# Kernel tuning notes

Hardware: AMD Instinct MI355X
Metric: run time of the kernel (lower is better)

Reference implementation:

```python
import jax, jax.numpy as jnp
import numpy as np

B, S, D, H = 4, 2048, 1024, 16
DH = D // H


def setup_inputs() -> dict:
    key = jax.random.key(0)
    ks = jax.random.split(key, 11)
    s = 1.0 / np.sqrt(D)
    return {
        "q": jax.random.normal(ks[0], (B, S, D), jnp.float32),
        "k": jax.random.normal(ks[1], (B, S, D), jnp.float32),
        "v": jax.random.normal(ks[2], (B, S, D), jnp.float32),
        "Wq": jax.random.normal(ks[3], (D, D), jnp.float32) * s,
        "bq": jnp.zeros((D,), jnp.float32),
        "Wk": jax.random.normal(ks[4], (D, D), jnp.float32) * s,
        "bk": jnp.zeros((D,), jnp.float32),
        "Wv": jax.random.normal(ks[5], (D, D), jnp.float32) * s,
        "bv": jnp.zeros((D,), jnp.float32),
        "Wo": jax.random.normal(ks[6], (D, D), jnp.float32) * s,
        "bo": jnp.zeros((D,), jnp.float32),
    }


def _split_heads(x):
    # (B, S, D) -> (B, H, S, DH)
    b, s, _ = x.shape
    return x.reshape(b, s, H, DH).transpose(0, 2, 1, 3)


def reference(q, k, v, Wq, bq, Wk, bk, Wv, bv, Wo, bo):
    # torch Linear: x @ W.T + b
    qh = _split_heads(q @ Wq.T + bq)
    kh = _split_heads(k @ Wk.T + bk)
    vh = _split_heads(v @ Wv.T + bv)
    scale = 1.0 / jnp.sqrt(jnp.asarray(DH, qh.dtype))
    scores = jnp.einsum("bhqd,bhkd->bhqk", qh, kh) * scale  # (B,H,S,S)
    probs = jax.nn.softmax(scores, axis=-1)
    ctx = jnp.einsum("bhqk,bhkd->bhqd", probs, vh)  # (B,H,S,DH)
    x = ctx.transpose(0, 2, 1, 3).reshape(q.shape[0], -1, D)
    return x @ Wo.T + bo
```

## Files before the change

kernel.cpp:

```cpp
#include <hip/hip_runtime.h>

typedef __bf16 bf16x8 __attribute__((ext_vector_type(8)));
typedef __bf16 bf16x4 __attribute__((ext_vector_type(4)));
typedef _Float16 f16x8 __attribute__((ext_vector_type(8)));
typedef _Float16 f16x4v __attribute__((ext_vector_type(4)));
typedef __fp16 fp16x2 __attribute__((ext_vector_type(2)));
typedef float f32x4 __attribute__((ext_vector_type(4)));
typedef float f32x16 __attribute__((ext_vector_type(16)));
typedef unsigned short u16;
typedef unsigned int u32;
typedef unsigned int u32x4 __attribute__((ext_vector_type(4)));

constexpr int Bc = 4, Sc = 2048, Dc = 1024, Hc = 16, DHc = 64;
constexpr int Mrows = Bc * Sc;
constexpr size_t MK = (size_t)Mrows * Dc;
constexpr size_t WK = (size_t)Dc * Dc;

__device__ __forceinline__ u16 f2bf(float f) {
  u32 u = __float_as_uint(f);
  u = (u + 0x7fffu + ((u >> 16) & 1u)) >> 16;
  return (u16)u;
}

#define LDSP(p) ((__attribute__((address_space(3))) void*)(p))
#define GLBP(p) ((const __attribute__((address_space(1))) void*)(p))

__global__ __launch_bounds__(256) void cvt3_kernel(const float* __restrict__ a,
                                                   const float* __restrict__ b,
                                                   const float* __restrict__ c,
                                                   ushort4* __restrict__ out, int n4) {
  const float4* in = (const float4*)(blockIdx.y == 0 ? a : blockIdx.y == 1 ? b : c);
  ushort4* o = out + (size_t)blockIdx.y * n4;
  int stride = gridDim.x * blockDim.x;
  for (int i = blockIdx.x * blockDim.x + threadIdx.x; i < n4; i += stride) {
    float4 v = in[i];
    ushort4 r;
    r.x = f2bf(v.x); r.y = f2bf(v.y); r.z = f2bf(v.z); r.w = f2bf(v.w);
    o[i] = r;
  }
}

__global__ __launch_bounds__(256) void cvt4_kernel(const float* __restrict__ a,
                                                   const float* __restrict__ b,
                                                   const float* __restrict__ c,
                                                   const float* __restrict__ d,
                                                   ushort4* __restrict__ out, int n4) {
  const float4* in = (const float4*)(blockIdx.y == 0 ? a : blockIdx.y == 1 ? b
                                     : blockIdx.y == 2 ? c : d);
  ushort4* o = out + (size_t)blockIdx.y * n4;
  int stride = gridDim.x * blockDim.x;
  for (int i = blockIdx.x * blockDim.x + threadIdx.x; i < n4; i += stride) {
    float4 v = in[i];
    ushort4 r;
    r.x = f2bf(v.x); r.y = f2bf(v.y); r.z = f2bf(v.z); r.w = f2bf(v.w);
    o[i] = r;
  }
}

template <int FUSED3>
__global__ __launch_bounds__(256, 2) void gemm8(const u16* __restrict__ A0,
                                                const u16* __restrict__ Bt0,
                                                const float* __restrict__ b0,
                                                const float* __restrict__ b1,
                                                const float* __restrict__ b2,
                                                void* __restrict__ out0) {
  constexpr int K = 1024, NT = 32;
  __shared__ u16 lds[3 * 12288];

  const int y = FUSED3 ? (int)blockIdx.y : 3;
  const u16* A = A0 + (FUSED3 ? (size_t)blockIdx.y * MK : 0);
  const u16* Bt = Bt0 + (FUSED3 ? (size_t)blockIdx.y * WK : 0);
  const float* bias = FUSED3 ? (y == 0 ? b0 : y == 1 ? b1 : b2) : b0;

  const int wg = (blockIdx.x & 7) * 32 + (blockIdx.x >> 3);
  const int tm = wg >> 3, tn = wg & 7;
  const int row0 = tm << 8, col0 = tn << 7;

  const int t_ = threadIdx.x, w = t_ >> 6, l = t_ & 63;
  const int wm = w >> 1, wn = w & 1;
  const int col = l & 31, hh = l >> 5;

  f32x16 acc[4][2] = {};

  auto stA = [&](int tile, int i) {
    u16* buf = &lds[(tile % 3) * 12288];
    const int c = w * 4 + i;
    const int r = c * 16 + (l >> 2);
    const int sg = (l & 3) ^ ((r >> 1) & 3);
    __builtin_amdgcn_global_load_lds(
        GLBP(A + (size_t)(row0 + r) * K + (tile << 5) + sg * 8),
        LDSP(buf + c * 512), 16, 0, 0);
  };
  auto stB = [&](int tile, int i) {
    u16* buf = &lds[(tile % 3) * 12288] + 8192;
    const int c = w * 2 + i;
    const int r = c * 16 + (l >> 2);
    const int sg = (l & 3) ^ ((r >> 1) & 3);
    __builtin_amdgcn_global_load_lds(
        GLBP(Bt + (size_t)(col0 + r) * K + (tile << 5) + sg * 8),
        LDSP(buf + c * 512), 16, 0, 0);
  };

  stA(0, 0); stA(0, 1); stA(0, 2); stA(0, 3); stB(0, 0); stB(0, 1);
  stA(1, 0); stA(1, 1); stA(1, 2); stA(1, 3); stB(1, 0); stB(1, 1);
  asm volatile("s_waitcnt vmcnt(6)" ::: "memory");
  __builtin_amdgcn_s_barrier();

#pragma unroll 1
  for (int t = 0; t < NT; ++t) {
    const u16* abuf = &lds[(t % 3) * 12288];
    const u16* bbuf = abuf + 8192;
    if (t + 2 < NT) {
      stA(t + 2, 0); stA(t + 2, 1); stA(t + 2, 2); stA(t + 2, 3);
      stB(t + 2, 0); stB(t + 2, 1);
    }
    bf16x8 af[2][4], bf[2][2];
#pragma unroll
    for (int kc = 0; kc < 2; ++kc) {
      const int g = kc * 2 + hh;
#pragma unroll
      for (int mb = 0; mb < 4; ++mb) {
        const int ar = wm * 128 + mb * 32 + col;
        af[kc][mb] = *(const bf16x8*)&abuf[ar * 32 + ((g ^ ((ar >> 1) & 3)) << 3)];
      }
#pragma unroll
      for (int nb = 0; nb < 2; ++nb) {
        const int br = wn * 64 + nb * 32 + col;
        bf[kc][nb] = *(const bf16x8*)&bbuf[br * 32 + ((g ^ ((br >> 1) & 3)) << 3)];
      }
    }
    __builtin_amdgcn_s_setprio(1);
#pragma unroll
    for (int kc = 0; kc < 2; ++kc)
#pragma unroll
      for (int mb = 0; mb < 4; ++mb)
#pragma unroll
        for (int nb = 0; nb < 2; ++nb)
          acc[mb][nb] = __builtin_amdgcn_mfma_f32_32x32x16_bf16(af[kc][mb], bf[kc][nb],
                                                               acc[mb][nb], 0, 0, 0);
    __builtin_amdgcn_s_setprio(0);
    if (t + 2 < NT)      asm volatile("s_waitcnt vmcnt(6)" ::: "memory");
    else if (t + 1 < NT) asm volatile("s_waitcnt vmcnt(0)" ::: "memory");
    __builtin_amdgcn_s_barrier();
  }

#pragma unroll
  for (int mb = 0; mb < 4; ++mb)
#pragma unroll
    for (int nb = 0; nb < 2; ++nb) {
      const int n = col0 + wn * 64 + nb * 32 + col;
      const float bv = bias[n];
      const int mbase = row0 + wm * 128 + mb * 32 + 4 * hh;
      if (y == 3) {
        float* O = (float*)out0;
#pragma unroll
        for (int r = 0; r < 16; ++r) {
          const int m = mbase + (r & 3) + 8 * (r >> 2);
          O[(size_t)m * Dc + n] = acc[mb][nb][r] + bv;
        }
      } else if (y == 2) {
        u16* Vt = (u16*)out0 + 2 * MK;
        const int h = n >> 6, dh = n & 63;
#pragma unroll
        for (int qg = 0; qg < 4; ++qg) {
          const int s0 = mbase + 8 * qg;
          const int b = s0 >> 11, s = s0 & (Sc - 1);
          f16x4v pk;
#pragma unroll
          for (int r4 = 0; r4 < 4; ++r4) pk[r4] = (_Float16)(acc[mb][nb][qg * 4 + r4] + bv);
          *(f16x4v*)&Vt[((size_t)((b * Hc + h) * DHc + dh)) * Sc + s] = pk;
        }
      } else {
        u16* Oh = (u16*)out0 + (size_t)y * MK;
        const float scl = (y == 0) ? 0.125f * 1.44269504089f : 1.f;
        const int h = n >> 6, dh = n & 63;
#pragma unroll
        for (int r = 0; r < 16; ++r) {
          const int m = mbase + (r & 3) + 8 * (r >> 2);
          const int b = m >> 11, s = m & (Sc - 1);
          Oh[((size_t)((b * Hc + h) * Sc + s)) * DHc + dh] = f2bf((acc[mb][nb][r] + bv) * scl);
        }
      }
    }
}

__global__ __launch_bounds__(256, 4) void attn5_kernel(const u16* __restrict__ Qh,
                                                       const u16* __restrict__ Kh,
                                                       const u16* __restrict__ Vt,
                                                       u16* __restrict__ ctx) {
  __shared__ u16 smem[16384];
  u16* K_lds = smem;
  u16* V_lds = smem + 8192;

  const int wid = (blockIdx.x & 7) * 128 + (blockIdx.x >> 3);
  const int qt = wid & 15, bh = wid >> 4;
  const int t = threadIdx.x, w = t >> 6, l = t & 63;
  const int q = l & 31, h = l >> 5;
  const int q0 = qt * 128 + w * 32;

  bf16x8 qf[4];
  {
    const u16* qp = Qh + ((size_t)bh * Sc + q0 + q) * DHc + h * 8;
#pragma unroll
    for (int kk = 0; kk < 4; ++kk) qf[kk] = *(const bf16x8*)(qp + kk * 16);
  }

  f32x16 oacc[2] = {};
  float l_run = 0.f;
  const fp16x2 ones2 = {(__fp16)1.f, (__fp16)1.f};

  const int lrow = l >> 3, lg = l & 7;

  auto stage = [&](int tile, int buf) {
    const int kt = tile << 6;
    u16* Kb = K_lds + buf * 4096;
    u16* Vb = V_lds + buf * 4096;
#pragma unroll
    for (int c = 0; c < 2; ++c) {
      const int rb = w * 16 + c * 8;
      const int row = rb + lrow;
      const int sg = lg ^ (row & 7);
      __builtin_amdgcn_global_load_lds(GLBP(Kh + ((size_t)bh * Sc + kt + row) * DHc + sg * 8),
                                       LDSP(&Kb[rb * 64]), 16, 0, 0);
      __builtin_amdgcn_global_load_lds(GLBP(Vt + ((size_t)bh * DHc + row) * Sc + kt + sg * 8),
                                       LDSP(&Vb[rb * 64]), 16, 0, 0);
    }
  };

  stage(0, 0);
  __syncthreads();

#pragma unroll 1
  for (int tile = 0; tile < 32; ++tile) {
    const int cur = tile & 1;
    if (tile + 1 < 32) stage(tile + 1, cur ^ 1);
    const u16* Kb = K_lds + cur * 4096;
    const u16* Vb = V_lds + cur * 4096;

    f32x16 sacc[2] = {};
    __builtin_amdgcn_s_setprio(1);
#pragma unroll
    for (int kk = 0; kk < 4; ++kk) {
      const int kr0 = q, kr1 = 32 + q;
      bf16x8 kf0 = *(const bf16x8*)&Kb[kr0 * 64 + ((2 * kk + h) ^ (kr0 & 7)) * 8];
      bf16x8 kf1 = *(const bf16x8*)&Kb[kr1 * 64 + ((2 * kk + h) ^ (kr1 & 7)) * 8];
      sacc[0] = __builtin_amdgcn_mfma_f32_32x32x16_bf16(kf0, qf[kk], sacc[0], 0, 0, 0);
      sacc[1] = __builtin_amdgcn_mfma_f32_32x32x16_bf16(kf1, qf[kk], sacc[1], 0, 0, 0);
    }
    __builtin_amdgcn_s_setprio(0);

    float sumA = 0.f, sumB = 0.f;
#pragma unroll
    for (int kt32 = 0; kt32 < 2; ++kt32)
#pragma unroll
      for (int c = 0; c < 2; ++c) {
        float p0 = __builtin_amdgcn_exp2f(sacc[kt32][c * 8 + 0]);
        float p1 = __builtin_amdgcn_exp2f(sacc[kt32][c * 8 + 1]);
        float p2 = __builtin_amdgcn_exp2f(sacc[kt32][c * 8 + 2]);
        float p3 = __builtin_amdgcn_exp2f(sacc[kt32][c * 8 + 3]);
        float p4 = __builtin_amdgcn_exp2f(sacc[kt32][c * 8 + 4]);
        float p5 = __builtin_amdgcn_exp2f(sacc[kt32][c * 8 + 5]);
        float p6 = __builtin_amdgcn_exp2f(sacc[kt32][c * 8 + 6]);
        float p7 = __builtin_amdgcn_exp2f(sacc[kt32][c * 8 + 7]);
        fp16x2 X0 = __builtin_amdgcn_cvt_pkrtz(p0, p1);
        fp16x2 X1 = __builtin_amdgcn_cvt_pkrtz(p2, p3);
        fp16x2 Y0 = __builtin_amdgcn_cvt_pkrtz(p4, p5);
        fp16x2 Y1 = __builtin_amdgcn_cvt_pkrtz(p6, p7);
        sumA = __builtin_amdgcn_fdot2(X0, ones2, sumA, false);
        sumA = __builtin_amdgcn_fdot2(X1, ones2, sumA, false);
        sumB = __builtin_amdgcn_fdot2(Y0, ones2, sumB, false);
        sumB = __builtin_amdgcn_fdot2(Y1, ones2, sumB, false);
        auto rA = __builtin_amdgcn_permlane32_swap(__builtin_bit_cast(u32, X0),
                                                   __builtin_bit_cast(u32, Y0), false, false);
        auto rB = __builtin_amdgcn_permlane32_swap(__builtin_bit_cast(u32, X1),
                                                   __builtin_bit_cast(u32, Y1), false, false);
        u32x4 wv;
        wv[0] = rA[0]; wv[1] = rB[0]; wv[2] = rA[1]; wv[3] = rB[1];
        f16x8 pf = __builtin_bit_cast(f16x8, wv);
        const int gb = kt32 * 4 + c * 2 + h;
        __builtin_amdgcn_s_setprio(1);
#pragma unroll
        for (int dt = 0; dt < 2; ++dt) {
          const int vrow = dt * 32 + q;
          f16x8 vf = *(const f16x8*)&Vb[vrow * 64 + ((gb ^ (vrow & 7)) * 8)];
          oacc[dt] = __builtin_amdgcn_mfma_f32_32x32x16_f16(vf, pf, oacc[dt], 0, 0, 0);
        }
        __builtin_amdgcn_s_setprio(0);
      }
    l_run += sumA + sumB;
    __syncthreads();
  }

  l_run += __shfl_xor(l_run, 32);
  const float inv = 1.f / l_run;
  u16* E = smem + w * 2048;
#pragma unroll
  for (int dt = 0; dt < 2; ++dt)
#pragma unroll
    for (int rg = 0; rg < 4; ++rg) {
      bf16x4 pk;
#pragma unroll
      for (int j = 0; j < 4; ++j) pk[j] = (__bf16)(oacc[dt][rg * 4 + j] * inv);
      const int dh0 = dt * 32 + rg * 8 + 4 * h;
      int byte = q * 128 + dh0 * 2;
      byte ^= (q & 7) << 4;
      *(bf16x4*)((char*)E + byte) = pk;
    }
  __syncthreads();
  const int b = bh >> 4, head = bh & 15;
  const size_t crow = ((size_t)(b * Sc + q0 + q)) * Dc + head * 64 + h * 32;
#pragma unroll
  for (int i = 0; i < 4; ++i) {
    const int g = (4 * h + i) ^ (q & 7);
    uint4 tv = *(const uint4*)((char*)E + q * 128 + g * 16);
    *(uint4*)((u16*)ctx + crow + i * 8) = tv;
  }
}

extern "C" void kernel_launch(void* const* d_in, const int* in_sizes, int n_in,
                              void* d_out, int out_size, void* d_ws, size_t ws_size,
                              hipStream_t stream) {
  const float* q  = (const float*)d_in[0];
  const float* k  = (const float*)d_in[1];
  const float* v  = (const float*)d_in[2];
  const float* Wq = (const float*)d_in[3];
  const float* bq = (const float*)d_in[4];
  const float* Wk = (const float*)d_in[5];
  const float* bk = (const float*)d_in[6];
  const float* Wv = (const float*)d_in[7];
  const float* bv = (const float*)d_in[8];
  const float* Wo = (const float*)d_in[9];
  const float* bo = (const float*)d_in[10];
  float* out = (float*)d_out;

  u16* qb  = (u16*)d_ws;
  u16* Wqb = qb + 3 * MK;
  u16* Qh  = Wqb + 4 * WK;
  u16* Kh  = Qh + MK;
  u16* VtB = Kh + MK;
  u16* ctx = VtB + MK;

  cvt3_kernel<<<dim3(2048, 3), 256, 0, stream>>>(q, k, v, (ushort4*)qb, (int)(MK / 4));
  cvt4_kernel<<<dim3(512, 4), 256, 0, stream>>>(Wq, Wk, Wv, Wo, (ushort4*)Wqb, (int)(WK / 4));

  gemm8<1><<<dim3(256, 3), 256, 0, stream>>>(qb, Wqb, bq, bk, bv, (void*)Qh);

  attn5_kernel<<<1024, 256, 0, stream>>>(Qh, Kh, VtB, ctx);

  gemm8<0><<<dim3(256, 1), 256, 0, stream>>>(ctx, Wqb + 3 * WK, bo, bo, bo, (void*)out);
}
```

Before: 210.7 us.

## Fuse fp32-to-bf16 activation conversion into the QKV projection GEMM

Drops the separate kernel that converted q, k and v to bf16. The QKV GEMM now loads fp32 A tiles into registers, converts them with packed bf16 instructions and writes them to swizzled LDS, software-pipelined one tile ahead. B tiles still go through direct global-to-LDS loads. This removes a full write and re-read of three bf16 activation tensors, but doubles the A-side global read bytes inside the GEMM and adds register pressure and VALU work to its main loop.

```diff
diff --git a/kernel.cpp b/kernel.cpp
--- a/kernel.cpp
+++ b/kernel.cpp
@@ -24,21 +24,6 @@
 
 #define LDSP(p) ((__attribute__((address_space(3))) void*)(p))
 #define GLBP(p) ((const __attribute__((address_space(1))) void*)(p))
-
-__global__ __launch_bounds__(256) void cvt3_kernel(const float* __restrict__ a,
-                                                   const float* __restrict__ b,
-                                                   const float* __restrict__ c,
-                                                   ushort4* __restrict__ out, int n4) {
-  const float4* in = (const float4*)(blockIdx.y == 0 ? a : blockIdx.y == 1 ? b : c);
-  ushort4* o = out + (size_t)blockIdx.y * n4;
-  int stride = gridDim.x * blockDim.x;
-  for (int i = blockIdx.x * blockDim.x + threadIdx.x; i < n4; i += stride) {
-    float4 v = in[i];
-    ushort4 r;
-    r.x = f2bf(v.x); r.y = f2bf(v.y); r.z = f2bf(v.z); r.w = f2bf(v.w);
-    o[i] = r;
-  }
-}
 
 __global__ __launch_bounds__(256) void cvt4_kernel(const float* __restrict__ a,
                                                    const float* __restrict__ b,
@@ -57,20 +42,155 @@
   }
 }
 
-template <int FUSED3>
-__global__ __launch_bounds__(256, 2) void gemm8(const u16* __restrict__ A0,
-                                                const u16* __restrict__ Bt0,
-                                                const float* __restrict__ b0,
-                                                const float* __restrict__ b1,
-                                                const float* __restrict__ b2,
-                                                void* __restrict__ out0) {
+__global__ __launch_bounds__(256, 2) void gemmqkv(const float* __restrict__ Aq,
+                                                  const float* __restrict__ Ak,
+                                                  const float* __restrict__ Av,
+                                                  const u16* __restrict__ Bt0,
+                                                  const float* __restrict__ b0,
+                                                  const float* __restrict__ b1,
+                                                  const float* __restrict__ b2,
+                                                  void* __restrict__ out0) {
   constexpr int K = 1024, NT = 32;
   __shared__ u16 lds[3 * 12288];
 
-  const int y = FUSED3 ? (int)blockIdx.y : 3;
-  const u16* A = A0 + (FUSED3 ? (size_t)blockIdx.y * MK : 0);
-  const u16* Bt = Bt0 + (FUSED3 ? (size_t)blockIdx.y * WK : 0);
-  const float* bias = FUSED3 ? (y == 0 ? b0 : y == 1 ? b1 : b2) : b0;
+  const int y = blockIdx.y;
+  const float* A = (y == 0) ? Aq : (y == 1) ? Ak : Av;
+  const u16* Bt = Bt0 + (size_t)y * WK;
+  const float* bias = (y == 0) ? b0 : (y == 1) ? b1 : b2;
+
+  const int wg = (blockIdx.x & 7) * 32 + (blockIdx.x >> 3);
+  const int tm = wg >> 3, tn = wg & 7;
+  const int row0 = tm << 8, col0 = tn << 7;
+
+  const int t_ = threadIdx.x, w = t_ >> 6, l = t_ & 63;
+  const int wm = w >> 1, wn = w & 1;
+  const int col = l & 31, hh = l >> 5;
+
+  f32x16 acc[4][2] = {};
+  float4 areg[8];
+
+  auto ldA = [&](int tile) {
+#pragma unroll
+    for (int i = 0; i < 4; ++i) {
+      const int r = (w * 4 + i) * 16 + (l >> 2);
+      const float* p = A + (size_t)(row0 + r) * K + (tile << 5) + (l & 3) * 8;
+      areg[2 * i] = *(const float4*)p;
+      areg[2 * i + 1] = *(const float4*)(p + 4);
+    }
+  };
+  auto wrA = [&](int tile) {
+    u16* buf = &lds[(tile % 3) * 12288];
+#pragma unroll
+    for (int i = 0; i < 4; ++i) {
+      const int r = (w * 4 + i) * 16 + (l >> 2);
+      u32 d0, d1, d2, d3;
+      asm("v_cvt_pk_bf16_f32 %0, %1, %2" : "=v"(d0) : "v"(areg[2 * i].x), "v"(areg[2 * i].y));
+      asm("v_cvt_pk_bf16_f32 %0, %1, %2" : "=v"(d1) : "v"(areg[2 * i].z), "v"(areg[2 * i].w));
+      asm("v_cvt_pk_bf16_f32 %0, %1, %2" : "=v"(d2) : "v"(areg[2 * i + 1].x), "v"(areg[2 * i + 1].y));
+      asm("v_cvt_pk_bf16_f32 %0, %1, %2" : "=v"(d3) : "v"(areg[2 * i + 1].z), "v"(areg[2 * i + 1].w));
+      u32x4 pk; pk[0] = d0; pk[1] = d1; pk[2] = d2; pk[3] = d3;
+      const int g = (l & 3) ^ ((r >> 1) & 3);
+      *(u32x4*)((char*)buf + r * 64 + g * 16) = pk;
+    }
+  };
+  auto stB = [&](int tile, int i) {
+    u16* buf = &lds[(tile % 3) * 12288] + 8192;
+    const int c = w * 2 + i;
+    const int r = c * 16 + (l >> 2);
+    const int sg = (l & 3) ^ ((r >> 1) & 3);
+    __builtin_amdgcn_global_load_lds(
+        GLBP(Bt + (size_t)(col0 + r) * K + (tile << 5) + sg * 8),
+        LDSP(buf + c * 512), 16, 0, 0);
+  };
+
+  ldA(0);
+  stB(0, 0); stB(0, 1);
+  stB(1, 0); stB(1, 1);
+  asm volatile("s_waitcnt vmcnt(2)" ::: "memory");
+  wrA(0);
+  ldA(1);
+  asm volatile("s_waitcnt lgkmcnt(0)" ::: "memory");
+  __builtin_amdgcn_s_barrier();
+
+#pragma unroll 1
+  for (int t = 0; t < NT; ++t) {
+    const u16* abuf = &lds[(t % 3) * 12288];
+    const u16* bbuf = abuf + 8192;
+    if (t + 2 < NT) { stB(t + 2, 0); stB(t + 2, 1); }
+    bf16x8 af[2][4], bf[2][2];
+#pragma unroll
+    for (int kc = 0; kc < 2; ++kc) {
+      const int g = kc * 2 + hh;
+#pragma unroll
+      for (int mb = 0; mb < 4; ++mb) {
+        const int ar = wm * 128 + mb * 32 + col;
+        af[kc][mb] = *(const bf16x8*)&abuf[ar * 32 + ((g ^ ((ar >> 1) & 3)) << 3)];
+      }
+#pragma unroll
+      for (int nb = 0; nb < 2; ++nb) {
+        const int br = wn * 64 + nb * 32 + col;
+        bf[kc][nb] = *(const bf16x8*)&bbuf[br * 32 + ((g ^ ((br >> 1) & 3)) << 3)];
+      }
+    }
+    __builtin_amdgcn_s_setprio(1);
+#pragma unroll
+    for (int kc = 0; kc < 2; ++kc)
+#pragma unroll
+      for (int mb = 0; mb < 4; ++mb)
+#pragma unroll
+        for (int nb = 0; nb < 2; ++nb)
+          acc[mb][nb] = __builtin_amdgcn_mfma_f32_32x32x16_bf16(af[kc][mb], bf[kc][nb],
+                                                               acc[mb][nb], 0, 0, 0);
+    __builtin_amdgcn_s_setprio(0);
+    if (t + 1 < NT) {
+      if (t + 2 < NT) asm volatile("s_waitcnt vmcnt(2)" ::: "memory");
+      else            asm volatile("s_waitcnt vmcnt(0)" ::: "memory");
+      wrA(t + 1);
+      if (t + 2 < NT) ldA(t + 2);
+    }
+    asm volatile("s_waitcnt lgkmcnt(0)" ::: "memory");
+    __builtin_amdgcn_s_barrier();
+  }
+
+#pragma unroll
+  for (int mb = 0; mb < 4; ++mb)
+#pragma unroll
+    for (int nb = 0; nb < 2; ++nb) {
+      const int n = col0 + wn * 64 + nb * 32 + col;
+      const float bv = bias[n];
+      const int mbase = row0 + wm * 128 + mb * 32 + 4 * hh;
+      if (y == 2) {
+        u16* Vt = (u16*)out0 + 2 * MK;
+        const int h = n >> 6, dh = n & 63;
+#pragma unroll
+        for (int qg = 0; qg < 4; ++qg) {
+          const int s0 = mbase + 8 * qg;
+          const int b = s0 >> 11, s = s0 & (Sc - 1);
+          f16x4v pk;
+#pragma unroll
+          for (int r4 = 0; r4 < 4; ++r4) pk[r4] = (_Float16)(acc[mb][nb][qg * 4 + r4] + bv);
+          *(f16x4v*)&Vt[((size_t)((b * Hc + h) * DHc + dh)) * Sc + s] = pk;
+        }
+      } else {
+        u16* Oh = (u16*)out0 + (size_t)y * MK;
+        const float scl = (y == 0) ? 0.125f * 1.44269504089f : 1.f;
+        const int h = n >> 6, dh = n & 63;
+#pragma unroll
+        for (int r = 0; r < 16; ++r) {
+          const int m = mbase + (r & 3) + 8 * (r >> 2);
+          const int b = m >> 11, s = m & (Sc - 1);
+          Oh[((size_t)((b * Hc + h) * Sc + s)) * DHc + dh] = f2bf((acc[mb][nb][r] + bv) * scl);
+        }
+      }
+    }
+}
+
+__global__ __launch_bounds__(256, 2) void gemmout(const u16* __restrict__ A,
+                                                  const u16* __restrict__ Bt,
+                                                  const float* __restrict__ bias,
+                                                  float* __restrict__ O) {
+  constexpr int K = 1024, NT = 32;
+  __shared__ u16 lds[3 * 12288];
 
   const int wg = (blockIdx.x & 7) * 32 + (blockIdx.x >> 3);
   const int tm = wg >> 3, tn = wg & 7;
@@ -151,35 +271,10 @@
       const int n = col0 + wn * 64 + nb * 32 + col;
       const float bv = bias[n];
       const int mbase = row0 + wm * 128 + mb * 32 + 4 * hh;
-      if (y == 3) {
-        float* O = (float*)out0;
-#pragma unroll
-        for (int r = 0; r < 16; ++r) {
-          const int m = mbase + (r & 3) + 8 * (r >> 2);
-          O[(size_t)m * Dc + n] = acc[mb][nb][r] + bv;
-        }
-      } else if (y == 2) {
-        u16* Vt = (u16*)out0 + 2 * MK;
-        const int h = n >> 6, dh = n & 63;
-#pragma unroll
-        for (int qg = 0; qg < 4; ++qg) {
-          const int s0 = mbase + 8 * qg;
-          const int b = s0 >> 11, s = s0 & (Sc - 1);
-          f16x4v pk;
-#pragma unroll
-          for (int r4 = 0; r4 < 4; ++r4) pk[r4] = (_Float16)(acc[mb][nb][qg * 4 + r4] + bv);
-          *(f16x4v*)&Vt[((size_t)((b * Hc + h) * DHc + dh)) * Sc + s] = pk;
-        }
-      } else {
-        u16* Oh = (u16*)out0 + (size_t)y * MK;
-        const float scl = (y == 0) ? 0.125f * 1.44269504089f : 1.f;
-        const int h = n >> 6, dh = n & 63;
-#pragma unroll
-        for (int r = 0; r < 16; ++r) {
-          const int m = mbase + (r & 3) + 8 * (r >> 2);
-          const int b = m >> 11, s = m & (Sc - 1);
-          Oh[((size_t)((b * Hc + h) * Sc + s)) * DHc + dh] = f2bf((acc[mb][nb][r] + bv) * scl);
-        }
+#pragma unroll
+      for (int r = 0; r < 16; ++r) {
+        const int m = mbase + (r & 3) + 8 * (r >> 2);
+        O[(size_t)m * Dc + n] = acc[mb][nb][r] + bv;
       }
     }
 }
@@ -333,19 +428,17 @@
   const float* bo = (const float*)d_in[10];
   float* out = (float*)d_out;
 
-  u16* qb  = (u16*)d_ws;
-  u16* Wqb = qb + 3 * MK;
+  u16* Wqb = (u16*)d_ws;
   u16* Qh  = Wqb + 4 * WK;
   u16* Kh  = Qh + MK;
   u16* VtB = Kh + MK;
   u16* ctx = VtB + MK;
 
-  cvt3_kernel<<<dim3(2048, 3), 256, 0, stream>>>(q, k, v, (ushort4*)qb, (int)(MK / 4));
   cvt4_kernel<<<dim3(512, 4), 256, 0, stream>>>(Wq, Wk, Wv, Wo, (ushort4*)Wqb, (int)(WK / 4));
 
-  gemm8<1><<<dim3(256, 3), 256, 0, stream>>>(qb, Wqb, bq, bk, bv, (void*)Qh);
+  gemmqkv<<<dim3(256, 3), 256, 0, stream>>>(q, k, v, Wqb, bq, bk, bv, (void*)Qh);
 
   attn5_kernel<<<1024, 256, 0, stream>>>(Qh, Kh, VtB, ctx);
 
-  gemm8<0><<<dim3(256, 1), 256, 0, stream>>>(ctx, Wqb + 3 * WK, bo, bo, bo, (void*)out);
-}
+  gemmout<<<256, 256, 0, stream>>>(ctx, Wqb + 3 * WK, bo, out);
+}
```

Result: faster. 200.2 us (-5.0%).
